# Performance work log

Measured on AMD Instinct MI355X. Metric: run time of the kernel, lower is better.

The kernel has to match this reference:

```python
import jax, jax.numpy as jnp
import numpy as np

HEADS = 4
DIM_HEAD = 32
SCALE = DIM_HEAD ** (-0.5)


def setup_inputs() -> dict:
    key = jax.random.key(0)
    k1, k2, k3, k4 = jax.random.split(key, 4)
    dim = 256
    hidden = HEADS * DIM_HEAD  # 128
    x = jax.random.normal(k1, (8, dim, 48, 48), dtype=jnp.float32)
    w_qkv = jax.random.normal(k2, (3 * hidden, dim), dtype=jnp.float32) * (dim ** -0.5)
    w_out = jax.random.normal(k3, (dim, hidden), dtype=jnp.float32) * (hidden ** -0.5)
    b_out = jax.random.normal(k4, (dim,), dtype=jnp.float32) * 0.01
    return {"x": x, "w_qkv": w_qkv, "w_out": w_out, "b_out": b_out}


def reference(x, w_qkv, w_out, b_out):
    b, c, h, w = x.shape
    n = h * w
    xf = x.reshape(b, c, n)                                  # [b, c, n]
    # 1x1 Conv1d (no bias) == pointwise linear over channels
    qkv = jnp.einsum('oc,bcn->bon', w_qkv, xf)               # [b, 3*hidden, n]
    q, k, v = jnp.split(qkv, 3, axis=1)                      # each [b, hidden, n]
    def to_heads(t):
        return t.reshape(b, HEADS, DIM_HEAD, n)              # b h d n
    q, k, v = to_heads(q) * SCALE, to_heads(k), to_heads(v)
    sim = jnp.einsum('bhdi,bhdj->bhij', q, k)                # [b, h, n, n]
    attn = jax.nn.softmax(sim, axis=-1)                      # stable (max-subtracted)
    out = jnp.einsum('bhij,bhdj->bhid', attn, v)             # [b, h, n, d]
    # 'b h (x y) d -> b (h d) x y'
    out = out.transpose(0, 1, 3, 2).reshape(b, HEADS * DIM_HEAD, n)
    y = jnp.einsum('oc,bcn->bon', w_out, out) + b_out[None, :, None]
    return y.reshape(b, c, h, w)
```

## Files before the change

### kernel.cpp

```cpp
#include <hip/hip_runtime.h>
#include <math.h>

#define NB    8
#define CDIM  256
#define NN    2304
#define NH    4
#define DH    32
#define HIDC  128
#define OC3   384
#define SCALE_LOG2E 0.25503524964550864f
#define SEG   2359296
#define LSEG  73728
#define PPARTS 4
#define JCHUNK 576
#define NITER  18

typedef short  bf16x8 __attribute__((ext_vector_type(8)));
typedef float  f32x4  __attribute__((ext_vector_type(4)));

__device__ __forceinline__ unsigned short f2bf(float f) {
    union { float f; unsigned u; } a; a.f = f;
    unsigned r = a.u + 0x7fffu + ((a.u >> 16) & 1u);
    return (unsigned short)(r >> 16);
}

__device__ __forceinline__ unsigned pack_trunc(float lo, float hi) {
    union { float f; unsigned u; } a, b; a.f = lo; b.f = hi;
    return (b.u & 0xFFFF0000u) | (a.u >> 16);
}

__device__ __forceinline__ float bflo(unsigned u) {
    union { unsigned u; float f; } c; c.u = u << 16; return c.f;
}
__device__ __forceinline__ float bfhi(unsigned u) {
    union { unsigned u; float f; } c; c.u = u & 0xFFFF0000u; return c.f;
}

__global__ __launch_bounds__(256) void qkv_proj_kernel(
    const float* __restrict__ x, const float* __restrict__ w,
    unsigned short* __restrict__ qt, unsigned short* __restrict__ kt,
    unsigned short* __restrict__ vtT)
{
    __shared__ unsigned short As[64 * 40];
    __shared__ unsigned short Bs[128 * 40];
    const int Lb   = (int)blockIdx.x;
    const int xcd  = Lb & 7;
    const int t    = Lb >> 3;
    const int so   = t % 6;
    const int gl   = t / 6;
    const int group = gl * 8 + xcd;
    const int nb   = group % 18;
    const int b    = group / 18;
    const int n0 = nb * 128;
    const int o0 = so * 64;
    const int sel = so >> 1;

    const int tid  = (int)threadIdx.x;
    const int wave = tid >> 6;
    const int lane = tid & 63;
    const int li   = lane & 15;
    const int g    = lane >> 4;
    const int wm = (wave & 1) * 32;
    const int wn = (wave >> 1) * 64;
    const float* xb = x + (size_t)b * CDIM * NN;

    const int aco = (tid & 7) * 4;
    const int aor = tid >> 3;
    const int n4  = (tid & 31) * 4;
    const int c4  = (tid >> 5) * 4;

    f32x4 acc[2][4];
#pragma unroll
    for (int i = 0; i < 2; ++i)
#pragma unroll
        for (int j = 0; j < 4; ++j) acc[i][j] = (f32x4){0.f, 0.f, 0.f, 0.f};

    float4 wv[2], xv[4];
#pragma unroll
    for (int r = 0; r < 2; ++r)
        wv[r] = *(const float4*)&w[(size_t)(o0 + aor + 32 * r) * CDIM + aco];
#pragma unroll
    for (int dd = 0; dd < 4; ++dd)
        xv[dd] = *(const float4*)&xb[(size_t)(c4 + dd) * NN + n0 + n4];

    for (int k0 = 0; k0 < CDIM; k0 += 32) {
        __syncthreads();
#pragma unroll
        for (int r = 0; r < 2; ++r) {
            uint2 pk;
            pk.x = (unsigned)f2bf(wv[r].x) | ((unsigned)f2bf(wv[r].y) << 16);
            pk.y = (unsigned)f2bf(wv[r].z) | ((unsigned)f2bf(wv[r].w) << 16);
            *(uint2*)&As[(aor + 32 * r) * 40 + aco] = pk;
        }
#pragma unroll
        for (int j = 0; j < 4; ++j) {
            uint2 pk;
            pk.x = (unsigned)f2bf(((const float*)&xv[0])[j])
                 | ((unsigned)f2bf(((const float*)&xv[1])[j]) << 16);
            pk.y = (unsigned)f2bf(((const float*)&xv[2])[j])
                 | ((unsigned)f2bf(((const float*)&xv[3])[j]) << 16);
            *(uint2*)&Bs[(n4 + j) * 40 + c4] = pk;
        }
        __syncthreads();

        const int kn = (k0 + 32 < CDIM) ? (k0 + 32) : k0;
#pragma unroll
        for (int r = 0; r < 2; ++r)
            wv[r] = *(const float4*)&w[(size_t)(o0 + aor + 32 * r) * CDIM + kn + aco];
#pragma unroll
        for (int dd = 0; dd < 4; ++dd)
            xv[dd] = *(const float4*)&xb[(size_t)(kn + c4 + dd) * NN + n0 + n4];

        bf16x8 af[2], bfr[4];
#pragma unroll
        for (int mt = 0; mt < 2; ++mt)
            af[mt] = *(const bf16x8*)&As[(wm + mt * 16 + li) * 40 + g * 8];
#pragma unroll
        for (int nt = 0; nt < 4; ++nt)
            bfr[nt] = *(const bf16x8*)&Bs[(wn + nt * 16 + li) * 40 + g * 8];
#pragma unroll
        for (int mt = 0; mt < 2; ++mt)
#pragma unroll
            for (int nt = 0; nt < 4; ++nt)
                acc[mt][nt] = __builtin_amdgcn_mfma_f32_16x16x32_bf16(
                    af[mt], bfr[nt], acc[mt][nt], 0, 0, 0);
    }

    if (sel < 2) {
        unsigned short* dst = (sel == 0) ? qt : kt;
        const float mul = (sel == 0) ? SCALE_LOG2E : 1.0f;
#pragma unroll
        for (int mt = 0; mt < 2; ++mt) {
            const int ob = o0 + wm + mt * 16 + g * 4;
            const int d0 = ob & 31;
            const int h  = (ob & 127) >> 5;
            const size_t bh = (size_t)(b * NH + h);
#pragma unroll
            for (int nt = 0; nt < 4; ++nt) {
                const int n = n0 + wn + nt * 16 + li;
                const f32x4 a = acc[mt][nt];
                uint2 pk;
                pk.x = (unsigned)f2bf(a[0] * mul) | ((unsigned)f2bf(a[1] * mul) << 16);
                pk.y = (unsigned)f2bf(a[2] * mul) | ((unsigned)f2bf(a[3] * mul) << 16);
                *(uint2*)&dst[(bh * NN + n) * DH + d0] = pk;
            }
        }
    } else {
#pragma unroll
        for (int mt = 0; mt < 2; ++mt) {
            const int ob = o0 + wm + mt * 16 + g * 4;
            const int d0 = ob & 31;
            const int h  = (ob & 127) >> 5;
            const size_t bh = (size_t)(b * NH + h);
#pragma unroll
            for (int nt = 0; nt < 4; ++nt) {
                const int n = n0 + wn + nt * 16 + li;
                const f32x4 a = acc[mt][nt];
#pragma unroll
                for (int r = 0; r < 4; ++r)
                    vtT[(bh * DH + d0 + r) * (size_t)NN + n] = f2bf(a[r]);
            }
        }
    }
}

__global__ __launch_bounds__(256) void attn_kernel(
    const unsigned short* __restrict__ qt, const unsigned short* __restrict__ kt,
    const unsigned short* __restrict__ vtT, unsigned short* __restrict__ Op,
    float* __restrict__ Lp)
{
    __shared__ unsigned short Pl[4][4][16 * 32];
    const int Lb  = (int)blockIdx.x;
    const int xcd = Lb & 7;
    const int t   = Lb >> 3;
    const int ib  = t % 9;
    const int grp = (t / 9) * 8 + xcd;
    const int bh  = grp >> 2;
    const int part = grp & 3;
    const int jbeg = part * JCHUNK;

    const int tid  = (int)threadIdx.x;
    const int wave = tid >> 6;
    const int lane = tid & 63;
    const int li   = lane & 15;
    const int g    = lane >> 4;
    const int i0   = ib * 256 + wave * 64;

    const unsigned short* qb = qt  + (size_t)bh * NN * DH;
    const unsigned short* kb = kt  + (size_t)bh * NN * DH;
    const unsigned short* vb = vtT + (size_t)bh * DH * NN;

    bf16x8 qfA = *(const bf16x8*)(qb + (size_t)(i0 + li) * DH + g * 8);
    bf16x8 qfB = *(const bf16x8*)(qb + (size_t)(i0 + 16 + li) * DH + g * 8);
    bf16x8 qfC = *(const bf16x8*)(qb + (size_t)(i0 + 32 + li) * DH + g * 8);
    bf16x8 qfD = *(const bf16x8*)(qb + (size_t)(i0 + 48 + li) * DH + g * 8);

    bf16x8 ones;
#pragma unroll
    for (int r = 0; r < 8; ++r) ones[r] = (short)0x3F80;

    f32x4 O0A = {0.f,0.f,0.f,0.f}, O1A = {0.f,0.f,0.f,0.f}, LsA = {0.f,0.f,0.f,0.f};
    f32x4 O0B = {0.f,0.f,0.f,0.f}, O1B = {0.f,0.f,0.f,0.f}, LsB = {0.f,0.f,0.f,0.f};
    f32x4 O0C = {0.f,0.f,0.f,0.f}, O1C = {0.f,0.f,0.f,0.f}, LsC = {0.f,0.f,0.f,0.f};
    f32x4 O0D = {0.f,0.f,0.f,0.f}, O1D = {0.f,0.f,0.f,0.f}, LsD = {0.f,0.f,0.f,0.f};

    unsigned short* plA = &Pl[wave][0][0];
    unsigned short* plB = &Pl[wave][1][0];
    unsigned short* plC = &Pl[wave][2][0];
    unsigned short* plD = &Pl[wave][3][0];
    const int sw  = li & 6;
    const int pw  = li * 32;
    const int wr0 = pw + ((g ^ sw) << 2);
    const int wr1 = pw + (((4 + g) ^ sw) << 2);
    const int rdo = pw + (((2 * g) ^ sw) << 2);

    const unsigned short* kp0 = kb + (size_t)(jbeg + li) * DH + g * 8;
    const unsigned short* kp1 = kp0 + 16 * DH;
    const unsigned short* vp0 = vb + (size_t)li * NN + jbeg + g * 8;
    const unsigned short* vp1 = vp0 + 16 * NN;

    bf16x8 kf0A = *(const bf16x8*)kp0;
    bf16x8 kf1A = *(const bf16x8*)kp1;
    bf16x8 vf0A = *(const bf16x8*)vp0;
    bf16x8 vf1A = *(const bf16x8*)vp1;
    bf16x8 kf0B = *(const bf16x8*)(kp0 + 32 * DH);
    bf16x8 kf1B = *(const bf16x8*)(kp1 + 32 * DH);
    bf16x8 vf0B = *(const bf16x8*)(vp0 + 32);
    bf16x8 vf1B = *(const bf16x8*)(vp1 + 32);
    kp0 += 64 * DH; kp1 += 64 * DH;
    vp0 += 64;      vp1 += 64;

#define ATTN_ITER(KF0, KF1, VF0, VF1)                                          \
    do {                                                                       \
        f32x4 z = {0.f, 0.f, 0.f, 0.f};                                        \
        f32x4 s0A = __builtin_amdgcn_mfma_f32_16x16x32_bf16(KF0, qfA, z, 0, 0, 0); \
        f32x4 s0B = __builtin_amdgcn_mfma_f32_16x16x32_bf16(KF0, qfB, z, 0, 0, 0); \
        f32x4 s0C = __builtin_amdgcn_mfma_f32_16x16x32_bf16(KF0, qfC, z, 0, 0, 0); \
        f32x4 s0D = __builtin_amdgcn_mfma_f32_16x16x32_bf16(KF0, qfD, z, 0, 0, 0); \
        f32x4 s1A = __builtin_amdgcn_mfma_f32_16x16x32_bf16(KF1, qfA, z, 0, 0, 0); \
        f32x4 s1B = __builtin_amdgcn_mfma_f32_16x16x32_bf16(KF1, qfB, z, 0, 0, 0); \
        f32x4 s1C = __builtin_amdgcn_mfma_f32_16x16x32_bf16(KF1, qfC, z, 0, 0, 0); \
        f32x4 s1D = __builtin_amdgcn_mfma_f32_16x16x32_bf16(KF1, qfD, z, 0, 0, 0); \
                                     \
        KF0 = *(const bf16x8*)kp0;                                             \
        KF1 = *(const bf16x8*)kp1;                                             \
        kp0 += 32 * DH; kp1 += 32 * DH;                                        \
        float p0A[4], p1A[4], p0B[4], p1B[4];                                  \
        float p0C[4], p1C[4], p0D[4], p1D[4];                                  \
        _Pragma("unroll")                                                      \
        for (int r = 0; r < 4; ++r) {                                          \
            p0A[r] = __builtin_amdgcn_exp2f(s0A[r]);                           \
            p1A[r] = __builtin_amdgcn_exp2f(s1A[r]);                           \
            p0B[r] = __builtin_amdgcn_exp2f(s0B[r]);                           \
            p1B[r] = __builtin_amdgcn_exp2f(s1B[r]);                           \
            p0C[r] = __builtin_amdgcn_exp2f(s0C[r]);                           \
            p1C[r] = __builtin_amdgcn_exp2f(s1C[r]);                           \
            p0D[r] = __builtin_amdgcn_exp2f(s0D[r]);                           \
            p1D[r] = __builtin_amdgcn_exp2f(s1D[r]);                           \
        }                                                                      \
        uint2 wa, wb;                                                          \
        wa.x = pack_trunc(p0A[0], p0A[1]);  wa.y = pack_trunc(p0A[2], p0A[3]); \
        wb.x = pack_trunc(p1A[0], p1A[1]);  wb.y = pack_trunc(p1A[2], p1A[3]); \
        *(uint2*)&plA[wr0] = wa;                                               \
        *(uint2*)&plA[wr1] = wb;                                               \
        wa.x = pack_trunc(p0B[0], p0B[1]);  wa.y = pack_trunc(p0B[2], p0B[3]); \
        wb.x = pack_trunc(p1B[0], p1B[1]);  wb.y = pack_trunc(p1B[2], p1B[3]); \
        *(uint2*)&plB[wr0] = wa;                                               \
        *(uint2*)&plB[wr1] = wb;                                               \
        wa.x = pack_trunc(p0C[0], p0C[1]);  wa.y = pack_trunc(p0C[2], p0C[3]); \
        wb.x = pack_trunc(p1C[0], p1C[1]);  wb.y = pack_trunc(p1C[2], p1C[3]); \
        *(uint2*)&plC[wr0] = wa;                                               \
        *(uint2*)&plC[wr1] = wb;                                               \
        wa.x = pack_trunc(p0D[0], p0D[1]);  wa.y = pack_trunc(p0D[2], p0D[3]); \
        wb.x = pack_trunc(p1D[0], p1D[1]);  wb.y = pack_trunc(p1D[2], p1D[3]); \
        *(uint2*)&plD[wr0] = wa;                                               \
        *(uint2*)&plD[wr1] = wb;                                               \
        bf16x8 pfA = *(const bf16x8*)&plA[rdo];                                \
        bf16x8 pfB = *(const bf16x8*)&plB[rdo];                                \
        bf16x8 pfC = *(const bf16x8*)&plC[rdo];                                \
        bf16x8 pfD = *(const bf16x8*)&plD[rdo];                                \
        O0A = __builtin_amdgcn_mfma_f32_16x16x32_bf16(VF0,  pfA, O0A, 0, 0, 0); \
        O0B = __builtin_amdgcn_mfma_f32_16x16x32_bf16(VF0,  pfB, O0B, 0, 0, 0); \
        O0C = __builtin_amdgcn_mfma_f32_16x16x32_bf16(VF0,  pfC, O0C, 0, 0, 0); \
        O0D = __builtin_amdgcn_mfma_f32_16x16x32_bf16(VF0,  pfD, O0D, 0, 0, 0); \
        O1A = __builtin_amdgcn_mfma_f32_16x16x32_bf16(VF1,  pfA, O1A, 0, 0, 0); \
        O1B = __builtin_amdgcn_mfma_f32_16x16x32_bf16(VF1,  pfB, O1B, 0, 0, 0); \
        O1C = __builtin_amdgcn_mfma_f32_16x16x32_bf16(VF1,  pfC, O1C, 0, 0, 0); \
        O1D = __builtin_amdgcn_mfma_f32_16x16x32_bf16(VF1,  pfD, O1D, 0, 0, 0); \
        LsA = __builtin_amdgcn_mfma_f32_16x16x32_bf16(ones, pfA, LsA, 0, 0, 0); \
        LsB = __builtin_amdgcn_mfma_f32_16x16x32_bf16(ones, pfB, LsB, 0, 0, 0); \
        LsC = __builtin_amdgcn_mfma_f32_16x16x32_bf16(ones, pfC, LsC, 0, 0, 0); \
        LsD = __builtin_amdgcn_mfma_f32_16x16x32_bf16(ones, pfD, LsD, 0, 0, 0); \
                                     \
        VF0 = *(const bf16x8*)vp0;                                             \
        VF1 = *(const bf16x8*)vp1;                                             \
        vp0 += 32; vp1 += 32;                                                  \
    } while (0)

#pragma unroll 1
    for (int it = 0; it < NITER; it += 2) {
        ATTN_ITER(kf0A, kf1A, vf0A, vf1A);
        ATTN_ITER(kf0B, kf1B, vf0B, vf1B);
    }
#undef ATTN_ITER

    unsigned short* obA = Op + (size_t)part * SEG + (size_t)bh * DH * NN + i0 + li;
    unsigned short* obB = obA + 16;
    unsigned short* obC = obA + 32;
    unsigned short* obD = obA + 48;
#pragma unroll
    for (int r = 0; r < 4; ++r) {
        obA[(size_t)(4 * g + r)      * NN] = f2bf(O0A[r]);
        obA[(size_t)(16 + 4 * g + r) * NN] = f2bf(O1A[r]);
        obB[(size_t)(4 * g + r)      * NN] = f2bf(O0B[r]);
        obB[(size_t)(16 + 4 * g + r) * NN] = f2bf(O1B[r]);
        obC[(size_t)(4 * g + r)      * NN] = f2bf(O0C[r]);
        obC[(size_t)(16 + 4 * g + r) * NN] = f2bf(O1C[r]);
        obD[(size_t)(4 * g + r)      * NN] = f2bf(O0D[r]);
        obD[(size_t)(16 + 4 * g + r) * NN] = f2bf(O1D[r]);
    }
    if (g == 0) {
        float* lpb = Lp + (size_t)part * LSEG + (size_t)bh * NN + i0 + li;
        lpb[0]  = LsA[0];
        lpb[16] = LsB[0];
        lpb[32] = LsC[0];
        lpb[48] = LsD[0];
    }
}

__global__ __launch_bounds__(256) void out_proj_kernel(
    const unsigned short* __restrict__ Op, const float* __restrict__ Lp,
    const float* __restrict__ w, const float* __restrict__ bias,
    float* __restrict__ y)
{
    __shared__ unsigned short As[64 * 40];
    __shared__ unsigned short Bs[128 * 40];
    __shared__ float Linv[4][128];
    const int Lb   = (int)blockIdx.x;
    const int xcd  = Lb & 7;
    const int t    = Lb >> 3;
    const int so   = t % 4;
    const int gl   = t / 4;
    const int group = gl * 8 + xcd;
    const int nb   = group % 18;
    const int b    = group / 18;
    const int n0 = nb * 128;
    const int o0 = so * 64;

    const int tid  = (int)threadIdx.x;
    const int wave = tid >> 6;
    const int lane = tid & 63;
    const int li   = lane & 15;
    const int g    = lane >> 4;
    const int wm = (wave & 1) * 32;
    const int wn = (wave >> 1) * 64;

    const int aco = (tid & 7) * 4;
    const int aor = tid >> 3;
    const int n4  = (tid & 31) * 4;
    const int d4  = (tid >> 5) * 4;

    {
        const int h = tid >> 6, nb2 = tid & 63;
#pragma unroll
        for (int half = 0; half < 2; ++half) {
            const int n = nb2 + 64 * half;
            float s = 0.f;
#pragma unroll
            for (int p = 0; p < PPARTS; ++p)
                s += Lp[(size_t)p * LSEG + (size_t)(b * NH + h) * NN + n0 + n];
            Linv[h][n] = 1.0f / s;
        }
    }

    f32x4 acc[2][4];
#pragma unroll
    for (int i = 0; i < 2; ++i)
#pragma unroll
        for (int j = 0; j < 4; ++j) acc[i][j] = (f32x4){0.f, 0.f, 0.f, 0.f};

    float4 wv[2];
    uint2  ov[PPARTS][4];
#pragma unroll
    for (int r = 0; r < 2; ++r)
        wv[r] = *(const float4*)&w[(size_t)(o0 + aor + 32 * r) * HIDC + aco];
    {
        const size_t bh0 = (size_t)(b * NH);
#pragma unroll
        for (int p = 0; p < PPARTS; ++p)
#pragma unroll
            for (int dd = 0; dd < 4; ++dd)
                ov[p][dd] = *(const uint2*)&Op[(size_t)p * SEG
                              + (bh0 * DH + d4 + dd) * (size_t)NN + n0 + n4];
    }

    for (int k0 = 0; k0 < HIDC; k0 += 32) {
        __syncthreads();
#pragma unroll
        for (int r = 0; r < 2; ++r) {
            uint2 pk;
            pk.x = (unsigned)f2bf(wv[r].x) | ((unsigned)f2bf(wv[r].y) << 16);
            pk.y = (unsigned)f2bf(wv[r].z) | ((unsigned)f2bf(wv[r].w) << 16);
            *(uint2*)&As[(aor + 32 * r) * 40 + aco] = pk;
        }
        const int h = k0 >> 5;
        {
            float s[4][4];
#pragma unroll
            for (int dd = 0; dd < 4; ++dd)
#pragma unroll
                for (int j = 0; j < 4; ++j) s[dd][j] = 0.f;
#pragma unroll
            for (int p = 0; p < PPARTS; ++p) {
#pragma unroll
                for (int dd = 0; dd < 4; ++dd) {
                    const uint2 u = ov[p][dd];
                    s[dd][0] += bflo(u.x); s[dd][1] += bfhi(u.x);
                    s[dd][2] += bflo(u.y); s[dd][3] += bfhi(u.y);
                }
            }
#pragma unroll
            for (int j = 0; j < 4; ++j) {
                const float lv = Linv[h][n4 + j];
                uint2 pk;
                pk.x = (unsigned)f2bf(s[0][j] * lv) | ((unsigned)f2bf(s[1][j] * lv) << 16);
                pk.y = (unsigned)f2bf(s[2][j] * lv) | ((unsigned)f2bf(s[3][j] * lv) << 16);
                *(uint2*)&Bs[(n4 + j) * 40 + d4] = pk;
            }
        }
        __syncthreads();

        const int kn = (k0 + 32 < HIDC) ? (k0 + 32) : k0;
        const size_t bhn = (size_t)(b * NH + (kn >> 5));
#pragma unroll
        for (int r = 0; r < 2; ++r)
            wv[r] = *(const float4*)&w[(size_t)(o0 + aor + 32 * r) * HIDC + kn + aco];
#pragma unroll
        for (int p = 0; p < PPARTS; ++p)
#pragma unroll
            for (int dd = 0; dd < 4; ++dd)
                ov[p][dd] = *(const uint2*)&Op[(size_t)p * SEG
                              + (bhn * DH + d4 + dd) * (size_t)NN + n0 + n4];

        bf16x8 af[2], bfr[4];
#pragma unroll
        for (int mt = 0; mt < 2; ++mt)
            af[mt] = *(const bf16x8*)&As[(wm + mt * 16 + li) * 40 + g * 8];
#pragma unroll
        for (int nt = 0; nt < 4; ++nt)
            bfr[nt] = *(const bf16x8*)&Bs[(wn + nt * 16 + li) * 40 + g * 8];
#pragma unroll
        for (int mt = 0; mt < 2; ++mt)
#pragma unroll
            for (int nt = 0; nt < 4; ++nt)
                acc[mt][nt] = __builtin_amdgcn_mfma_f32_16x16x32_bf16(
                    af[mt], bfr[nt], acc[mt][nt], 0, 0, 0);
    }

#pragma unroll
    for (int mt = 0; mt < 2; ++mt) {
        const int ob = o0 + wm + mt * 16 + g * 4;
        const float b0 = bias[ob], b1 = bias[ob + 1], b2 = bias[ob + 2], b3 = bias[ob + 3];
#pragma unroll
        for (int nt = 0; nt < 4; ++nt) {
            const int n = n0 + wn + nt * 16 + li;
            const f32x4 a = acc[mt][nt];
            float* yb = y + ((size_t)(b * CDIM + ob)) * NN + n;
            yb[0]              = a[0] + b0;
            yb[(size_t)NN]     = a[1] + b1;
            yb[(size_t)2 * NN] = a[2] + b2;
            yb[(size_t)3 * NN] = a[3] + b3;
        }
    }
}

extern "C" void kernel_launch(void* const* d_in, const int* in_sizes, int n_in,
                              void* d_out, int out_size, void* d_ws, size_t ws_size,
                              hipStream_t stream)
{
    (void)in_sizes; (void)n_in; (void)out_size; (void)ws_size;
    const float* x     = (const float*)d_in[0];
    const float* w_qkv = (const float*)d_in[1];
    const float* w_out = (const float*)d_in[2];
    const float* b_out = (const float*)d_in[3];
    float* y = (float*)d_out;

    unsigned short* qt  = (unsigned short*)d_ws;
    unsigned short* kt  = qt + SEG;
    unsigned short* vtT = kt + SEG;
    unsigned short* Op  = vtT + SEG;
    float* Lp = (float*)(Op + (size_t)PPARTS * SEG);

    qkv_proj_kernel<<<dim3(864), 256, 0, stream>>>(x, w_qkv, qt, kt, vtT);

    attn_kernel<<<dim3(1152), 256, 0, stream>>>(qt, kt, vtT, Op, Lp);

    out_proj_kernel<<<dim3(576), 256, 0, stream>>>(Op, Lp, w_out, b_out, y);
}
```

Measured before the change: 142.9 us.

## Fuse three kernels into one persistent kernel with grid barriers

Merges the QKV projection, attention and output projection kernels into a single persistent kernel of 576 blocks. The blocks loop over each stage's tasks and meet at atomic-counter grid barriers between stages. The aim is to remove the launch gaps and tail effects between the three separate launches. In exchange, task counts of 864 and 1152 no longer divide evenly over the grid, each stage waits for the slowest block, and a memset is added to reset the barrier counter. Co-residency of all 576 blocks is assumed (launch_bounds 256,3), otherwise the barrier deadlocks.

```diff
diff --git a/kernel.cpp b/kernel.cpp
--- a/kernel.cpp
+++ b/kernel.cpp
@@ -14,6 +14,7 @@
 #define PPARTS 4
 #define JCHUNK 576
 #define NITER  18
+#define GRID  576
 
 typedef short  bf16x8 __attribute__((ext_vector_type(8)));
 typedef float  f32x4  __attribute__((ext_vector_type(4)));
@@ -36,14 +37,24 @@
     union { unsigned u; float f; } c; c.u = u & 0xFFFF0000u; return c.f;
 }
 
-__global__ __launch_bounds__(256) void qkv_proj_kernel(
+__device__ __forceinline__ void grid_bar(unsigned* cnt, unsigned n) {
+    __syncthreads();
+    if (threadIdx.x == 0) {
+        __threadfence();
+        __hip_atomic_fetch_add(cnt, 1u, __ATOMIC_RELEASE, __HIP_MEMORY_SCOPE_AGENT);
+        while (__hip_atomic_load(cnt, __ATOMIC_ACQUIRE, __HIP_MEMORY_SCOPE_AGENT) < n)
+            __builtin_amdgcn_s_sleep(8);
+        __threadfence();
+    }
+    __syncthreads();
+}
+
+__device__ __forceinline__ void qkv_body(
+    int Lb, unsigned short* As, unsigned short* Bs,
     const float* __restrict__ x, const float* __restrict__ w,
     unsigned short* __restrict__ qt, unsigned short* __restrict__ kt,
     unsigned short* __restrict__ vtT)
 {
-    __shared__ unsigned short As[64 * 40];
-    __shared__ unsigned short Bs[128 * 40];
-    const int Lb   = (int)blockIdx.x;
     const int xcd  = Lb & 7;
     const int t    = Lb >> 3;
     const int so   = t % 6;
@@ -164,13 +175,12 @@
     }
 }
 
-__global__ __launch_bounds__(256) void attn_kernel(
+__device__ __forceinline__ void attn_body(
+    int Lb, unsigned short* Pl,
     const unsigned short* __restrict__ qt, const unsigned short* __restrict__ kt,
     const unsigned short* __restrict__ vtT, unsigned short* __restrict__ Op,
     float* __restrict__ Lp)
 {
-    __shared__ unsigned short Pl[4][4][16 * 32];
-    const int Lb  = (int)blockIdx.x;
     const int xcd = Lb & 7;
     const int t   = Lb >> 3;
     const int ib  = t % 9;
@@ -204,10 +214,10 @@
     f32x4 O0C = {0.f,0.f,0.f,0.f}, O1C = {0.f,0.f,0.f,0.f}, LsC = {0.f,0.f,0.f,0.f};
     f32x4 O0D = {0.f,0.f,0.f,0.f}, O1D = {0.f,0.f,0.f,0.f}, LsD = {0.f,0.f,0.f,0.f};
 
-    unsigned short* plA = &Pl[wave][0][0];
-    unsigned short* plB = &Pl[wave][1][0];
-    unsigned short* plC = &Pl[wave][2][0];
-    unsigned short* plD = &Pl[wave][3][0];
+    unsigned short* plA = Pl + wave * 2048;
+    unsigned short* plB = plA + 512;
+    unsigned short* plC = plA + 1024;
+    unsigned short* plD = plA + 1536;
     const int sw  = li & 6;
     const int pw  = li * 32;
     const int wr0 = pw + ((g ^ sw) << 2);
@@ -241,7 +251,6 @@
         f32x4 s1B = __builtin_amdgcn_mfma_f32_16x16x32_bf16(KF1, qfB, z, 0, 0, 0); \
         f32x4 s1C = __builtin_amdgcn_mfma_f32_16x16x32_bf16(KF1, qfC, z, 0, 0, 0); \
         f32x4 s1D = __builtin_amdgcn_mfma_f32_16x16x32_bf16(KF1, qfD, z, 0, 0, 0); \
-                                     \
         KF0 = *(const bf16x8*)kp0;                                             \
         KF1 = *(const bf16x8*)kp1;                                             \
         kp0 += 32 * DH; kp1 += 32 * DH;                                        \
@@ -291,7 +300,6 @@
         LsB = __builtin_amdgcn_mfma_f32_16x16x32_bf16(ones, pfB, LsB, 0, 0, 0); \
         LsC = __builtin_amdgcn_mfma_f32_16x16x32_bf16(ones, pfC, LsC, 0, 0, 0); \
         LsD = __builtin_amdgcn_mfma_f32_16x16x32_bf16(ones, pfD, LsD, 0, 0, 0); \
-                                     \
         VF0 = *(const bf16x8*)vp0;                                             \
         VF1 = *(const bf16x8*)vp1;                                             \
         vp0 += 32; vp1 += 32;                                                  \
@@ -328,15 +336,12 @@
     }
 }
 
-__global__ __launch_bounds__(256) void out_proj_kernel(
+__device__ __forceinline__ void out_body(
+    int Lb, unsigned short* As, unsigned short* Bs, float* Linv ,
     const unsigned short* __restrict__ Op, const float* __restrict__ Lp,
     const float* __restrict__ w, const float* __restrict__ bias,
     float* __restrict__ y)
 {
-    __shared__ unsigned short As[64 * 40];
-    __shared__ unsigned short Bs[128 * 40];
-    __shared__ float Linv[4][128];
-    const int Lb   = (int)blockIdx.x;
     const int xcd  = Lb & 7;
     const int t    = Lb >> 3;
     const int so   = t % 4;
@@ -369,7 +374,7 @@
 #pragma unroll
             for (int p = 0; p < PPARTS; ++p)
                 s += Lp[(size_t)p * LSEG + (size_t)(b * NH + h) * NN + n0 + n];
-            Linv[h][n] = 1.0f / s;
+            Linv[h * 128 + n] = 1.0f / s;
         }
     }
 
@@ -421,7 +426,7 @@
             }
 #pragma unroll
             for (int j = 0; j < 4; ++j) {
-                const float lv = Linv[h][n4 + j];
+                const float lv = Linv[h * 128 + n4 + j];
                 uint2 pk;
                 pk.x = (unsigned)f2bf(s[0][j] * lv) | ((unsigned)f2bf(s[1][j] * lv) << 16);
                 pk.y = (unsigned)f2bf(s[2][j] * lv) | ((unsigned)f2bf(s[3][j] * lv) << 16);
@@ -471,6 +476,41 @@
             yb[(size_t)2 * NN] = a[2] + b2;
             yb[(size_t)3 * NN] = a[3] + b3;
         }
+    }
+}
+
+__global__ __launch_bounds__(256, 3) void fused_kernel(
+    const float* __restrict__ x, const float* __restrict__ w_qkv,
+    const float* __restrict__ w_out, const float* __restrict__ b_out,
+    float* __restrict__ y,
+    unsigned short* qt, unsigned short* kt, unsigned short* vtT,
+    unsigned short* Op, float* Lp, unsigned* bar)
+{
+    __shared__ __align__(16) unsigned char smem[17664];
+    const int bid = (int)blockIdx.x;
+
+    {
+        unsigned short* As = (unsigned short*)smem;
+        unsigned short* Bs = As + 64 * 40;
+#pragma unroll 1
+        for (int task = bid; task < 864; task += GRID)
+            qkv_body(task, As, Bs, x, w_qkv, qt, kt, vtT);
+    }
+    grid_bar(&bar[0], GRID);
+    {
+        unsigned short* Pl = (unsigned short*)smem;
+#pragma unroll 1
+        for (int task = bid; task < 1152; task += GRID)
+            attn_body(task, Pl, qt, kt, vtT, Op, Lp);
+    }
+    grid_bar(&bar[8], GRID);
+    {
+        unsigned short* As = (unsigned short*)smem;
+        unsigned short* Bs = As + 64 * 40;
+        float* Linv = (float*)(Bs + 128 * 40);
+#pragma unroll 1
+        for (int task = bid; task < 576; task += GRID)
+            out_body(task, As, Bs, Linv, Op, Lp, w_out, b_out, y);
     }
 }
 
@@ -490,10 +530,10 @@
     unsigned short* vtT = kt + SEG;
     unsigned short* Op  = vtT + SEG;
     float* Lp = (float*)(Op + (size_t)PPARTS * SEG);
-
-    qkv_proj_kernel<<<dim3(864), 256, 0, stream>>>(x, w_qkv, qt, kt, vtT);
-
-    attn_kernel<<<dim3(1152), 256, 0, stream>>>(qt, kt, vtT, Op, Lp);
-
-    out_proj_kernel<<<dim3(576), 256, 0, stream>>>(Op, Lp, w_out, b_out, y);
-}
+    unsigned* bar = (unsigned*)(Lp + (size_t)PPARTS * LSEG);
+
+    hipMemsetAsync(bar, 0, 64, stream);
+
+    fused_kernel<<<dim3(GRID), 256, 0, stream>>>(
+        x, w_qkv, w_out, b_out, y, qt, kt, vtT, Op, Lp, bar);
+}
```

After: 500.0 us. 250% more time.
